# Kernel optimization log

Measured on AMD Instinct MI355X. Metric: run time of the kernel, lower is better.

Reference implementation:

```python
import jax, jax.numpy as jnp
import numpy as np

N_U = 16        # walkers per molecule
N_ORB = 12      # number of orbitals
N_FEAT = 14     # feature dim, fixed by w being 14x14
H1_THR = 0.0
H2_THR = 0.0


def setup_inputs() -> dict:
    key = jax.random.key(0)
    k1, k2, k3, k4, k5 = jax.random.split(key, 5)
    B = 16
    T = B * N_U  # 256 total walker samples
    mfv = jax.random.normal(k1, (T, N_ORB, N_FEAT), jnp.float32) * 0.1
    h1 = jax.random.normal(k2, (T, N_ORB, N_ORB), jnp.float32)
    h2 = jax.random.normal(k3, (T, N_ORB, N_ORB, N_ORB, N_ORB), jnp.float32)
    # occupancies in {1,2} so p_x_i determinants are generically nonzero
    V_n_hf = 1 + jax.random.randint(k4, (B, N_U, N_ORB), 0, 2, jnp.int32)
    w = jax.random.normal(k5, (N_FEAT, N_FEAT), jnp.float32) * 0.1
    return {"molec_feature_vectors": mfv, "h1": h1, "h2": h2,
            "V_n_hf": V_n_hf, "w": w}


def _forward(mfv, h1, h2, V_n_hf, w):
    T, n, f = mfv.shape
    B = T // N_U
    Vn = V_n_hf.reshape(T, n)                      # (T, n_orb) int occupancies

    eye = jnp.eye(n, dtype=jnp.int32)
    # c^dag c excitation patterns: (n, n^2)
    c1 = (eye[:, None, :] - eye[:, :, None]).reshape(n, n * n)
    # c^dag c^dag c c patterns: (n, n^4)
    c2 = (c1[:, None, :] - c1[:, :, None]).reshape(n, n ** 4)
    Wsym = w + w.T
    h1f = h1.reshape(T, n * n)
    h2f = h2.reshape(T, n ** 4)

    def per_sample(x, h1v, h2v, phi):
        # G[a,i] = phi[a] @ Wsym @ phi[i]; the c-sum inside calc_ampl factors as
        # det( G * (S S^T) ) because einsum('abc,bj,ijc->aic') keeps c aligned.
        G = phi @ Wsym @ phi.T                     # (n, n)

        # ---- one-body term ----
        s1 = c1 + x[:, None]                       # (n, n^2)
        m1 = ((s1.max(0) - s1.min(0)) == 1) & (h1v > H1_THR)
        s1f = s1.astype(phi.dtype) * m1            # boolean_mask -> zero columns
        det1 = jnp.linalg.det(G * (s1f @ s1f.T))
        e1 = det1 ** 2 * jnp.sum(jnp.where(m1, h1v, 0.0) ** 2)

        # ---- two-body term ----
        s2 = c2 + x[:, None]                       # (n, n^4)
        m2 = ((s2.max(0) - s2.min(0)) == 1) & (h2v > H2_THR)
        s2f = s2.astype(phi.dtype) * m2
        # reduce_sum over (orbital, feature) of phi[:, :, None] * s2[:, None, :]
        a2 = phi.sum(1) @ s2f                      # (n^4,)
        e2 = jnp.sum((jnp.where(m2, h2v, 0.0) * a2) ** 2)

        # ---- sampling probability of current state ----
        xf = x.astype(phi.dtype)
        p = jnp.linalg.det(G * jnp.outer(xf, xf)) ** 2
        return e1 + e2, p

    e, p = jax.vmap(per_sample)(Vn, h1f, h2f, mfv)
    e = e.reshape(B, N_U)
    p = p.reshape(B, N_U)
    return jnp.sum(e * p, axis=1) / jnp.sum(p, axis=1)   # (B,)


def reference(molec_feature_vectors, h1, h2, V_n_hf, w):
    return _forward(molec_feature_vectors, h1, h2, V_n_hf, w)
```

## Files before the change

kernel.cpp:

```cpp
#include <hip/hip_runtime.h>

#define NORB   12
#define NFEAT  14
#define NCOL1  144
#define NCOL2  20736
#define RPB    192
#define NSPLIT 9
#define CPS    (NSPLIT + 1)
#define NT     256

extern "C" __global__ void __launch_bounds__(RPB)
eloc_fused(const float* __restrict__ mfv, const float* __restrict__ h1,
           const float* __restrict__ h2, const int* __restrict__ vn,
           const float* __restrict__ w,
           double* __restrict__ ep, double* __restrict__ part)
{
    const int tid = threadIdx.x;
    const int bid = blockIdx.x;
    const int t   = bid / CPS;
    const int ch  = bid % CPS;

    __shared__ float phi_s[NORB][NFEAT];
    __shared__ float ps_s[NORB];
    __shared__ int   x_s[NORB];
    __shared__ float Sv_s;
    __shared__ float W_s[NFEAT][NFEAT];
    __shared__ float tmp_s[NORB][NFEAT];
    __shared__ float G_s[NORB][NORB];
    __shared__ unsigned char m1_s[NCOL1];
    __shared__ int Ri_s[NORB], Rj_s[NORB], M_s;
    __shared__ double A1[NORB][NORB], A2[NORB][NORB];
    __shared__ double red_s[RPB / 64];
    __shared__ double det_s[2];
    __shared__ double h1sum_s;

    if (tid < NORB * NFEAT)
        phi_s[tid / NFEAT][tid % NFEAT] = mfv[(size_t)t * NORB * NFEAT + tid];
    if (tid >= NORB * NFEAT && tid < NORB * NFEAT + NORB)
        x_s[tid - NORB * NFEAT] = vn[t * NORB + (tid - NORB * NFEAT)];
    __syncthreads();
    if (tid < NORB) {
        float s = 0.f;
        #pragma unroll
        for (int f = 0; f < NFEAT; ++f) s += phi_s[tid][f];
        ps_s[tid] = s;
    }
    __syncthreads();
    if (tid == 0) {
        float s = 0.f;
        for (int a = 0; a < NORB; ++a) s += ps_s[a] * (float)x_s[a];
        Sv_s = s;
    }
    __syncthreads();

    int X2 = 0;
    #pragma unroll
    for (int a = 0; a < NORB; ++a) X2 |= (x_s[a] == 2) ? (1 << a) : 0;
    const int nx2 = ~X2 & 0xFFF;
    const float Sv = Sv_s;

    if (ch != 0) {
        float psv[NORB];
        #pragma unroll
        for (int q = 0; q < NORB; ++q) psv[q] = ps_s[q];

        const int r = (ch - 1) * RPB + tid;
        const int i = r / 144, j = (r / NORB) % NORB, p = r % NORB;

        const float4* hr = (const float4*)(h2 + (size_t)t * NCOL2 + (size_t)r * NORB);
        const float4 ha = hr[0], hb = hr[1], hc = hr[2];

        const int bi = 1 << i, bj = 1 << j, bp = 1 << p;
        const int um0 = 0xFFF & ~(bi | bj | bp);
        const int xi = 1 + ((X2 >> i) & 1);
        const int xj = 1 + ((X2 >> j) & 1);
        const int xp = 1 + ((X2 >> p) & 1);
        const int basei = xi + 1 - ((bi >> j) & 1) - ((bi >> p) & 1);
        const int basej = xj + ((bj >> i) & 1) - 1 - ((bj >> p) & 1);
        const int basep = xp + ((bp >> i) & 1) - ((bp >> j) & 1) - 1;
        const float a2b = Sv + psv[i] - psv[j] - psv[p];

        float acc = 0.f;
#define COLQ(q, hv) {                                                       \
        const int bq  = 1 << (q);                                           \
        const int um  = um0 & ~bq;                                          \
        const int hm1 = nx2 & um, hm2 = X2 & um;                            \
        int mn = hm1 ? 1 : (hm2 ? 2 : 9);                                   \
        int mx = hm2 ? 2 : (hm1 ? 1 : -9);                                  \
        const int iq = (bi >> (q)) & 1, jq = (bj >> (q)) & 1,               \
                  pq = (bp >> (q)) & 1;                                     \
        const int vi = basei + iq, vj = basej + jq, vp = basep + pq;        \
        const int xq = 1 + ((X2 >> (q)) & 1);                               \
        const int vq = xq + 1 + iq - jq - pq;                               \
        mn = min(min(mn, vi), min(vj, min(vp, vq)));                        \
        mx = max(max(mx, vi), max(vj, max(vp, vq)));                        \
        const bool ok = (mx - mn == 1) && ((hv) > 0.0f);                    \
        const float tq = ok ? (hv) * (a2b + psv[q]) : 0.0f;                 \
        acc = fmaf(tq, tq, acc);                                            \
    }
        COLQ(0,  ha.x)  COLQ(1,  ha.y)  COLQ(2,  ha.z)  COLQ(3,  ha.w)
        COLQ(4,  hb.x)  COLQ(5,  hb.y)  COLQ(6,  hb.z)  COLQ(7,  hb.w)
        COLQ(8,  hc.x)  COLQ(9,  hc.y)  COLQ(10, hc.z)  COLQ(11, hc.w)
#undef COLQ

        double accd = (double)acc;
        #pragma unroll
        for (int o = 32; o > 0; o >>= 1) accd += __shfl_down(accd, o, 64);
        const int wv = tid >> 6, lane = tid & 63;
        if (lane == 0) red_s[wv] = accd;
        __syncthreads();
        if (tid == 0) part[t * NSPLIT + (ch - 1)] = red_s[0] + red_s[1] + red_s[2];
    } else {
        for (int k2 = tid; k2 < NFEAT * NFEAT; k2 += RPB) {
            int r2 = k2 / NFEAT, c2 = k2 % NFEAT;
            W_s[r2][c2] = w[k2] + w[c2 * NFEAT + r2];
        }
        __syncthreads();
        if (tid < NORB * NFEAT) {
            int a = tid / NFEAT, f = tid % NFEAT;
            float s = 0.f;
            #pragma unroll
            for (int g = 0; g < NFEAT; ++g) s += phi_s[a][g] * W_s[g][f];
            tmp_s[a][f] = s;
        }
        __syncthreads();
        if (tid < NCOL1) {
            int a = tid / NORB, i = tid % NORB;
            float s = 0.f;
            #pragma unroll
            for (int f = 0; f < NFEAT; ++f) s += tmp_s[a][f] * phi_s[i][f];
            G_s[a][i] = s;
        }

        double h1c = 0.0;
        if (tid < NCOL1) {
            int ii = tid / NORB, jj = tid % NORB;
            int um  = 0xFFF & ~((1 << ii) | (1 << jj));
            int hm1 = nx2 & um, hm2 = X2 & um;
            int mn = hm1 ? 1 : (hm2 ? 2 : 9);
            int mx = hm2 ? 2 : (hm1 ? 1 : -9);
            int d  = (ii == jj) ? 0 : 1;
            int vi = x_s[ii] - d, vj = x_s[jj] + d;
            mn = min(mn, min(vi, vj));
            mx = max(mx, max(vi, vj));
            float h1v = h1[(size_t)t * NCOL1 + tid];
            bool ok = (mx - mn == 1) && (h1v > 0.0f);
            m1_s[tid] = ok ? 1 : 0;
            if (ok) h1c = (double)h1v * (double)h1v;
        }
        __syncthreads();
        {
            #pragma unroll
            for (int o = 32; o > 0; o >>= 1) h1c += __shfl_down(h1c, o, 64);
            const int wv = tid >> 6, lane = tid & 63;
            if (lane == 0) red_s[wv] = h1c;
            __syncthreads();
            if (tid == 0) h1sum_s = red_s[0] + red_s[1] + red_s[2];
        }

        if (tid < NORB) {
            int ri = 0, rj = 0;
            #pragma unroll
            for (int o = 0; o < NORB; ++o) {
                ri += m1_s[tid * NORB + o];
                rj += m1_s[o * NORB + tid];
            }
            Ri_s[tid] = ri;
            Rj_s[tid] = rj;
        }
        __syncthreads();
        if (tid == 0) {
            int m = 0;
            #pragma unroll
            for (int o = 0; o < NORB; ++o) m += Ri_s[o];
            M_s = m;
        }
        __syncthreads();

        if (tid < NCOL1) {
            int a = tid / NORB, b = tid % NORB;
            int xa = x_s[a], xb = x_s[b];
            int Da = Rj_s[a] - Ri_s[a], Db = Rj_s[b] - Ri_s[b];
            int s1 = xa * xb * M_s + xa * Db + xb * Da
                   - (int)m1_s[b * NORB + a] - (int)m1_s[a * NORB + b];
            if (a == b) s1 += Rj_s[a] + Ri_s[a];
            A1[a][b] = (double)G_s[a][b] * (double)s1;
            A2[a][b] = (double)G_s[a][b];
        }
        __syncthreads();

        const int wv = tid >> 6, lane = tid & 63;
        if (wv < 2) {
            const double* Abase = (wv == 0) ? &A1[0][0] : &A2[0][0];
            const int rl = (lane < NORB) ? lane : 0;
            double a[NORB];
            #pragma unroll
            for (int c = 0; c < NORB; ++c) a[c] = Abase[rl * NORB + c];
            double det = 1.0;
            #pragma unroll
            for (int k = 0; k < NORB; ++k) {
                double key = (lane >= k && lane < NORB) ? fabs(a[k]) : -1.0;
                int idx = lane;
                #pragma unroll
                for (int off = 8; off >= 1; off >>= 1) {
                    double k2 = __shfl_xor(key, off);
                    int    i2 = __shfl_xor(idx, off);
                    if (k2 > key || (k2 == key && i2 < idx)) { key = k2; idx = i2; }
                }
                int pr = idx;
                if (pr != k) det = -det;
                int src = (lane == k) ? pr : ((lane == pr) ? k : lane);
                #pragma unroll
                for (int c = 0; c < NORB; ++c) a[c] = __shfl(a[c], src);
                double pk[NORB];
                #pragma unroll
                for (int c = 0; c < NORB; ++c) pk[c] = __shfl(a[c], k);
                double piv = pk[k];
                det *= piv;
                double inv = (piv != 0.0) ? 1.0 / piv : 0.0;
                double f = (lane > k && lane < NORB) ? a[k] * inv : 0.0;
                #pragma unroll
                for (int c = 0; c < NORB; ++c) a[c] = fma(-f, pk[c], a[c]);
            }
            if (lane == 0) det_s[wv] = det;
        }
        __syncthreads();

        if (tid == 0) {
            double e1 = det_s[0] * det_s[0] * h1sum_s;
            int n2 = __popc(X2);
            double pd = det_s[1] * (double)(1ull << (2 * n2));
            ep[2 * t]     = e1;
            ep[2 * t + 1] = pd * pd;
        }
    }
}

extern "C" __global__ void __launch_bounds__(256)
eloc_final(const double* __restrict__ ep, const double* __restrict__ part,
           float* __restrict__ out)
{
    const int s = threadIdx.x;
    __shared__ double se_s[NT], sp_s[NT];
    if (s < NT) {
        double e2 = 0.0;
        #pragma unroll
        for (int k = 0; k < NSPLIT; ++k) e2 += part[s * NSPLIT + k];
        double e = ep[2 * s] + e2;
        double p = ep[2 * s + 1];
        se_s[s] = e * p;
        sp_s[s] = p;
    }
    __syncthreads();
    if (s < NT / 16) {
        double se = 0.0, sp = 0.0;
        #pragma unroll
        for (int u = 0; u < 16; ++u) {
            se += se_s[s * 16 + u];
            sp += sp_s[s * 16 + u];
        }
        out[s] = (float)(se / sp);
    }
}

extern "C" void kernel_launch(void* const* d_in, const int* in_sizes, int n_in,
                              void* d_out, int out_size, void* d_ws, size_t ws_size,
                              hipStream_t stream) {
    const float* mfv = (const float*)d_in[0];
    const float* h1  = (const float*)d_in[1];
    const float* h2  = (const float*)d_in[2];
    const int*   vn  = (const int*)d_in[3];
    const float* w   = (const float*)d_in[4];
    float* out = (float*)d_out;

    double* ep   = (double*)d_ws;
    double* part = ep + 2 * NT;

    hipLaunchKernelGGL(eloc_fused, dim3(NT * CPS), dim3(RPB), 0, stream,
                       mfv, h1, h2, vn, w, ep, part);
    hipLaunchKernelGGL(eloc_final, dim3(1), dim3(256), 0, stream, ep, part, out);
}
```

Baseline: 25.08 us.

## Make h2 blocks barrier-free with wave-local prep and per-wave partial sums

Blocks that handle the two-body columns no longer stage phi and occupancies in shared memory. Each wave now loads its own row sums and occupancies, builds the doubly-occupied mask with a ballot, and reduces Sv with shuffles. Each wave writes its own partial sum straight to global memory, and the final kernel sums three times as many partials. This removes every __syncthreads from those blocks. The cost is redundant per-wave global loads of the row sums and a partial buffer that must now be three times larger, which the host allocation code may not provide.

```diff
diff --git a/kernel.cpp b/kernel.cpp
--- a/kernel.cpp
+++ b/kernel.cpp
@@ -8,6 +8,7 @@
 #define NSPLIT 9
 #define CPS    (NSPLIT + 1)
 #define NT     256
+#define WPS    (NSPLIT * 3)
 
 extern "C" __global__ void __launch_bounds__(RPB)
 eloc_fused(const float* __restrict__ mfv, const float* __restrict__ h1,
@@ -21,9 +22,7 @@
     const int ch  = bid % CPS;
 
     __shared__ float phi_s[NORB][NFEAT];
-    __shared__ float ps_s[NORB];
     __shared__ int   x_s[NORB];
-    __shared__ float Sv_s;
     __shared__ float W_s[NFEAT][NFEAT];
     __shared__ float tmp_s[NORB][NFEAT];
     __shared__ float G_s[NORB][NORB];
@@ -34,41 +33,38 @@
     __shared__ double det_s[2];
     __shared__ double h1sum_s;
 
-    if (tid < NORB * NFEAT)
-        phi_s[tid / NFEAT][tid % NFEAT] = mfv[(size_t)t * NORB * NFEAT + tid];
-    if (tid >= NORB * NFEAT && tid < NORB * NFEAT + NORB)
-        x_s[tid - NORB * NFEAT] = vn[t * NORB + (tid - NORB * NFEAT)];
-    __syncthreads();
-    if (tid < NORB) {
-        float s = 0.f;
-        #pragma unroll
-        for (int f = 0; f < NFEAT; ++f) s += phi_s[tid][f];
-        ps_s[tid] = s;
-    }
-    __syncthreads();
-    if (tid == 0) {
-        float s = 0.f;
-        for (int a = 0; a < NORB; ++a) s += ps_s[a] * (float)x_s[a];
-        Sv_s = s;
-    }
-    __syncthreads();
-
-    int X2 = 0;
-    #pragma unroll
-    for (int a = 0; a < NORB; ++a) X2 |= (x_s[a] == 2) ? (1 << a) : 0;
-    const int nx2 = ~X2 & 0xFFF;
-    const float Sv = Sv_s;
-
     if (ch != 0) {
-        float psv[NORB];
-        #pragma unroll
-        for (int q = 0; q < NORB; ++q) psv[q] = ps_s[q];
-
+        const int lane = tid & 63, wvi = tid >> 6;
         const int r = (ch - 1) * RPB + tid;
         const int i = r / 144, j = (r / NORB) % NORB, p = r % NORB;
 
         const float4* hr = (const float4*)(h2 + (size_t)t * NCOL2 + (size_t)r * NORB);
         const float4 ha = hr[0], hb = hr[1], hc = hr[2];
+
+        int   xv  = 1;
+        float psl = 0.f;
+        if (lane < NORB) {
+            xv = vn[t * NORB + lane];
+            const float* pr = mfv + (size_t)t * NORB * NFEAT + lane * NFEAT;
+            float s = 0.f;
+            #pragma unroll
+            for (int f = 0; f < NFEAT; ++f) s += pr[f];
+            psl = s;
+        }
+        const unsigned long long bal = __ballot(xv == 2);
+        const int X2  = (int)(bal & 0xFFFull);
+        const int nx2 = ~X2 & 0xFFF;
+
+        float sv = (lane < NORB) ? psl * (float)xv : 0.f;
+        sv += __shfl_xor(sv, 8, 16);
+        sv += __shfl_xor(sv, 4, 16);
+        sv += __shfl_xor(sv, 2, 16);
+        sv += __shfl_xor(sv, 1, 16);
+        const float Sv = __shfl(sv, 0, 64);
+
+        float psv[NORB];
+        #pragma unroll
+        for (int q = 0; q < NORB; ++q) psv[q] = __shfl(psl, q, 64);
 
         const int bi = 1 << i, bj = 1 << j, bp = 1 << p;
         const int um0 = 0xFFF & ~(bi | bj | bp);
@@ -78,7 +74,8 @@
         const int basei = xi + 1 - ((bi >> j) & 1) - ((bi >> p) & 1);
         const int basej = xj + ((bj >> i) & 1) - 1 - ((bj >> p) & 1);
         const int basep = xp + ((bp >> i) & 1) - ((bp >> j) & 1) - 1;
-        const float a2b = Sv + psv[i] - psv[j] - psv[p];
+        const float a2b = Sv + __shfl(psl, i, 64) - __shfl(psl, j, 64)
+                        - __shfl(psl, p, 64);
 
         float acc = 0.f;
 #define COLQ(q, hv) {                                                       \
@@ -106,16 +103,23 @@
         double accd = (double)acc;
         #pragma unroll
         for (int o = 32; o > 0; o >>= 1) accd += __shfl_down(accd, o, 64);
-        const int wv = tid >> 6, lane = tid & 63;
-        if (lane == 0) red_s[wv] = accd;
-        __syncthreads();
-        if (tid == 0) part[t * NSPLIT + (ch - 1)] = red_s[0] + red_s[1] + red_s[2];
+        if (lane == 0) part[t * WPS + (ch - 1) * 3 + wvi] = accd;
     } else {
+        if (tid < NORB * NFEAT)
+            phi_s[tid / NFEAT][tid % NFEAT] = mfv[(size_t)t * NORB * NFEAT + tid];
+        if (tid >= NORB * NFEAT && tid < NORB * NFEAT + NORB)
+            x_s[tid - NORB * NFEAT] = vn[t * NORB + (tid - NORB * NFEAT)];
         for (int k2 = tid; k2 < NFEAT * NFEAT; k2 += RPB) {
             int r2 = k2 / NFEAT, c2 = k2 % NFEAT;
             W_s[r2][c2] = w[k2] + w[c2 * NFEAT + r2];
         }
         __syncthreads();
+
+        int X2 = 0;
+        #pragma unroll
+        for (int a = 0; a < NORB; ++a) X2 |= (x_s[a] == 2) ? (1 << a) : 0;
+        const int nx2 = ~X2 & 0xFFF;
+
         if (tid < NORB * NFEAT) {
             int a = tid / NFEAT, f = tid % NFEAT;
             float s = 0.f;
@@ -152,8 +156,8 @@
         {
             #pragma unroll
             for (int o = 32; o > 0; o >>= 1) h1c += __shfl_down(h1c, o, 64);
-            const int wv = tid >> 6, lane = tid & 63;
-            if (lane == 0) red_s[wv] = h1c;
+            const int wvv = tid >> 6, lane = tid & 63;
+            if (lane == 0) red_s[wvv] = h1c;
             __syncthreads();
             if (tid == 0) h1sum_s = red_s[0] + red_s[1] + red_s[2];
         }
@@ -189,9 +193,9 @@
         }
         __syncthreads();
 
-        const int wv = tid >> 6, lane = tid & 63;
-        if (wv < 2) {
-            const double* Abase = (wv == 0) ? &A1[0][0] : &A2[0][0];
+        const int wvv = tid >> 6, lane = tid & 63;
+        if (wvv < 2) {
+            const double* Abase = (wvv == 0) ? &A1[0][0] : &A2[0][0];
             const int rl = (lane < NORB) ? lane : 0;
             double a[NORB];
             #pragma unroll
@@ -222,7 +226,7 @@
                 #pragma unroll
                 for (int c = 0; c < NORB; ++c) a[c] = fma(-f, pk[c], a[c]);
             }
-            if (lane == 0) det_s[wv] = det;
+            if (lane == 0) det_s[wvv] = det;
         }
         __syncthreads();
 
@@ -245,7 +249,7 @@
     if (s < NT) {
         double e2 = 0.0;
         #pragma unroll
-        for (int k = 0; k < NSPLIT; ++k) e2 += part[s * NSPLIT + k];
+        for (int k = 0; k < WPS; ++k) e2 += part[s * WPS + k];
         double e = ep[2 * s] + e2;
         double p = ep[2 * s + 1];
         se_s[s] = e * p;
```

Result: no change. 25.19 us (+0.4%).
